# Optimization experiments

Hardware: AMD Instinct MI355X
Metric: run time of the kernel (lower is better)

## Reference

```python
import jax, jax.numpy as jnp
import numpy as np

B = 65536   # batch
S = 3       # pad_size / seq len
DIN = 72    # input feature dim
D = 100     # dim_model
H = 10      # num_head
DH = D // H # dim_head = 10
FF = 512    # ffn hidden
L = 8       # encoder layers
CLS = 40    # cls_dim


def _pos_encoding():
    pe = np.array([[pos / 10000.0 ** (i // 2 * 2.0 / D) for i in range(D)]
                   for pos in range(S)], dtype=np.float32)
    pe[:, 0::2] = np.sin(pe[:, 0::2])
    pe[:, 1::2] = np.cos(pe[:, 1::2])
    return jnp.asarray(pe)  # [S, D]


def setup_inputs() -> dict:
    key = jax.random.key(0)
    ks = jax.random.split(key, 24)
    n = lambda k, shape: 0.05 * jax.random.normal(k, shape, dtype=jnp.float32)
    inp = {
        'x': jax.random.normal(ks[0], (B, S, DIN), dtype=jnp.float32),
        'label': jax.random.randint(ks[1], (B,), 0, CLS),
        'fa_label': jax.random.randint(ks[2], (B,), 0, CLS),
        'We': n(ks[3], (D, DIN)), 'be': n(ks[4], (D,)),
        'pe': _pos_encoding(),
        'Wq': n(ks[5], (L, D, D)), 'bq': n(ks[6], (L, D)),
        'Wk': n(ks[7], (L, D, D)), 'bk': n(ks[8], (L, D)),
        'Wv': n(ks[9], (L, D, D)), 'bv': n(ks[10], (L, D)),
        'Wo': n(ks[11], (L, D, D)), 'bo': n(ks[12], (L, D)),
        'ln1_g': jnp.ones((L, D), jnp.float32), 'ln1_b': jnp.zeros((L, D), jnp.float32),
        'W1': n(ks[13], (L, FF, D)), 'b1': n(ks[14], (L, FF)),
        'W2': n(ks[15], (L, D, FF)), 'b2': n(ks[16], (L, D)),
        'ln2_g': jnp.ones((L, D), jnp.float32), 'ln2_b': jnp.zeros((L, D), jnp.float32),
        'Wf': n(ks[17], (CLS, S * D)), 'bf': n(ks[18], (CLS,)),
    }
    return inp


def _ln(x, g, b, eps=1e-5):
    m = x.mean(-1, keepdims=True)
    v = ((x - m) ** 2).mean(-1, keepdims=True)
    return (x - m) / jnp.sqrt(v + eps) * g + b


def _forward(x, We, be, pe, Wq, bq, Wk, bk, Wv, bv, Wo, bo,
             ln1_g, ln1_b, W1, b1, W2, b2, ln2_g, ln2_b, Wf, bf):
    Bsz = x.shape[0]
    out = x @ We.T + be          # [B, S, D] embedding
    out = out + pe               # positional encoding (dropout = identity in eval)
    scale = DH ** -0.5
    for i in range(L):
        xin = out
        Q = xin @ Wq[i].T + bq[i]
        K = xin @ Wk[i].T + bk[i]
        V = xin @ Wv[i].T + bv[i]
        # Faithful row-major reshape (original uses .view, which interleaves
        # seq and head dims rather than a transpose-based head split).
        Qh = Q.reshape(Bsz * H, -1, DH)   # [B*H, S, DH]
        Kh = K.reshape(Bsz * H, -1, DH)
        Vh = V.reshape(Bsz * H, -1, DH)
        attn = jax.nn.softmax(jnp.einsum('bqd,bkd->bqk', Qh, Kh) * scale, axis=-1)
        ctx = jnp.einsum('bqk,bkd->bqd', attn, Vh).reshape(Bsz, -1, D)
        out = _ln(ctx @ Wo[i].T + bo[i] + xin, ln1_g[i], ln1_b[i])
        # position-wise FFN
        h = jax.nn.relu(out @ W1[i].T + b1[i])
        out = _ln(h @ W2[i].T + b2[i] + out, ln2_g[i], ln2_b[i])
    out = out.reshape(Bsz, S * D) @ Wf.T + bf   # [B, CLS]
    return out


def reference(x, label, fa_label, We, be, pe, Wq, bq, Wk, bk, Wv, bv, Wo, bo,
              ln1_g, ln1_b, W1, b1, W2, b2, ln2_g, ln2_b, Wf, bf):
    # label / fa_label are unused in the original forward
    return _forward(x, We, be, pe, Wq, bq, Wk, bk, Wv, bv, Wo, bo,
                    ln1_g, ln1_b, W1, b1, W2, b2, ln2_g, ln2_b, Wf, bf)
```

## Files before the change

kernel.cpp:

```cpp
#include <hip/hip_runtime.h>
#include <hip/hip_bf16.h>


typedef __attribute__((ext_vector_type(8))) short short8;
typedef __attribute__((ext_vector_type(4))) float floatx4;

namespace {
constexpr int S = 3, DIN = 72, D = 100, FF = 512, L = 8, CLS = 40;
constexpr int NB = 16, R = 48, NT = 256;
constexpr int LDA = 136;
constexpr int LDH = 200;
constexpr float SCALE_L2E = 0.45622024f;

constexpr int PL_QKVO = 7 * 4 * 512;
constexpr int WQ_OFF = 0;
constexpr int WK_OFF = WQ_OFF + L * PL_QKVO;
constexpr int WV_OFF = WK_OFF + L * PL_QKVO;
constexpr int WO_OFF = WV_OFF + L * PL_QKVO;
constexpr int PL_W1 = 32 * 4 * 512;
constexpr int W1_OFF = WO_OFF + L * PL_QKVO;
constexpr int PL_W2 = 7 * 16 * 512;
constexpr int W2_OFF = W1_OFF + L * PL_W1;
constexpr int WE_OFF = W2_OFF + L * PL_W2;
}

__device__ __forceinline__ unsigned short f2bf(float f) {
  unsigned int u = __float_as_uint(f);
  u = u + 0x7fffu + ((u >> 16) & 1u);
  return (unsigned short)(u >> 16);
}

__device__ __forceinline__ unsigned pkbf(float a, float b) {
  __hip_bfloat162 h = __float22bfloat162_rn(make_float2(a, b));
  return *reinterpret_cast<unsigned*>(&h);
}

__device__ __forceinline__ void st_bf4(unsigned short* p, floatx4 v) {
  *reinterpret_cast<uint2*>(p) = make_uint2(pkbf(v.x, v.y), pkbf(v.z, v.w));
}

__device__ __forceinline__ void load10(float* o, const unsigned short* p) {
  const unsigned* u = (const unsigned*)p;
#pragma unroll
  for (int w = 0; w < 5; ++w) {
    unsigned x = u[w];
    o[2 * w] = __uint_as_float(x << 16);
    o[2 * w + 1] = __uint_as_float(x & 0xffff0000u);
  }
}

__device__ __forceinline__ void ldwf4(const unsigned short* base, short8* o) {
#pragma unroll
  for (int ks = 0; ks < 4; ++ks) o[ks] = *(const short8*)(base + ks * 512);
}

__device__ __forceinline__ void ln_rows(float* xrow, const float* srow,
                                        const float* __restrict__ g,
                                        const float* __restrict__ b,
                                        unsigned short* sArow, int ln,
                                        int cnt) {
  floatx4 v[7];
  float sum = 0.f;
#pragma unroll
  for (int i = 0; i < 7; ++i)
    if (i < cnt) {
      const int col = i * 16 + ln * 4;
      floatx4 t = *(const floatx4*)(xrow + col) + *(const floatx4*)(srow + col);
      v[i] = t;
      sum += t.x + t.y + t.z + t.w;
    }
  sum += __shfl_xor(sum, 1, 4);
  sum += __shfl_xor(sum, 2, 4);
  const float mean = sum * 0.01f;
  float var = 0.f;
#pragma unroll
  for (int i = 0; i < 7; ++i)
    if (i < cnt) {
      floatx4 d = v[i] - mean;
      var += d.x * d.x + d.y * d.y + d.z * d.z + d.w * d.w;
    }
  var += __shfl_xor(var, 1, 4);
  var += __shfl_xor(var, 2, 4);
  const float rstd = rsqrtf(var * 0.01f + 1e-5f);
#pragma unroll
  for (int i = 0; i < 7; ++i)
    if (i < cnt) {
      const int col = i * 16 + ln * 4;
      floatx4 o = (v[i] - mean) * rstd * *(const floatx4*)(g + col) +
                  *(const floatx4*)(b + col);
      *(floatx4*)(xrow + col) = o;
      st_bf4(sArow + col, o);
    }
}

__global__ void prep_weights(const float* __restrict__ Wq, const float* __restrict__ Wk,
                             const float* __restrict__ Wv, const float* __restrict__ Wo,
                             const float* __restrict__ W1, const float* __restrict__ W2,
                             const float* __restrict__ We,
                             unsigned short* __restrict__ ws) {
  const int gid = blockIdx.x * 256 + threadIdx.x;
  constexpr int T_QKVO = 8 * 7 * 4 * 64;
  constexpr int T_W1 = 8 * 32 * 4 * 64;
  constexpr int T_W2 = 8 * 7 * 16 * 64;
  constexpr int T_WE = 7 * 3 * 64;
  if (gid >= 4 * T_QKVO + T_W1 + T_W2 + T_WE) return;

  const float* src;
  unsigned short* dst;
  int within, ntc, ksc, N, Ksrc, lstride;
  if (gid < 4 * T_QKVO) {
    const int t = gid / T_QKVO;
    within = gid % T_QKVO;
    src = (t == 0 ? Wq : t == 1 ? Wk : t == 2 ? Wv : Wo);
    dst = ws + (t == 0 ? WQ_OFF : t == 1 ? WK_OFF : t == 2 ? WV_OFF : WO_OFF);
    ntc = 7; ksc = 4; N = 100; Ksrc = 100; lstride = 10000;
  } else if (gid < 4 * T_QKVO + T_W1) {
    within = gid - 4 * T_QKVO;
    src = W1; dst = ws + W1_OFF;
    ntc = 32; ksc = 4; N = 512; Ksrc = 100; lstride = 51200;
  } else if (gid < 4 * T_QKVO + T_W1 + T_W2) {
    within = gid - 4 * T_QKVO - T_W1;
    src = W2; dst = ws + W2_OFF;
    ntc = 7; ksc = 16; N = 100; Ksrc = 512; lstride = 51200;
  } else {
    within = gid - 4 * T_QKVO - T_W1 - T_W2;
    src = We; dst = ws + WE_OFF;
    ntc = 7; ksc = 3; N = 100; Ksrc = 72; lstride = 0;
  }
  const int lane = within & 63;
  int tmp = within >> 6;
  const int ks = tmp % ksc; tmp /= ksc;
  const int nt = tmp % ntc;
  const int lay = tmp / ntc;
  const int n = nt * 16 + (lane & 15);
  const int kb = ks * 32 + (lane >> 4) * 8;
  const float* sp = src + (size_t)lay * lstride + (size_t)n * Ksrc;
  unsigned short o[8];
#pragma unroll
  for (int j = 0; j < 8; ++j) {
    const int k = kb + j;
    float v = (n < N && k < Ksrc) ? sp[k] : 0.f;
    o[j] = f2bf(v);
  }
  uint4 pk = make_uint4((unsigned)o[0] | ((unsigned)o[1] << 16),
                        (unsigned)o[2] | ((unsigned)o[3] << 16),
                        (unsigned)o[4] | ((unsigned)o[5] << 16),
                        (unsigned)o[6] | ((unsigned)o[7] << 16));
  *reinterpret_cast<uint4*>(dst + (size_t)within * 8) = pk;
}

__global__ __launch_bounds__(NT, 3)
void geomap_mfma(const float* __restrict__ gx,
                 const float* __restrict__ be, const float* __restrict__ pe,
                 const float* __restrict__ bq, const float* __restrict__ bk,
                 const float* __restrict__ bv, const float* __restrict__ bo,
                 const float* __restrict__ g1, const float* __restrict__ bt1,
                 const float* __restrict__ b1, const float* __restrict__ b2,
                 const float* __restrict__ g2, const float* __restrict__ bt2,
                 const float* __restrict__ Wf, const float* __restrict__ bfc,
                 const unsigned short* __restrict__ ws,
                 float* __restrict__ gout) {
  __shared__ __align__(16) char smem[51456];
  unsigned short* sA = (unsigned short*)smem;
  float* sXf = (float*)(smem + 13056);
  unsigned short* sQ = (unsigned short*)(smem + 32256);
  unsigned short* sK = (unsigned short*)(smem + 41856);
  float* scr = (float*)(smem + 32256);
  unsigned short* sH = (unsigned short*)(smem + 32256);

  const int tid = threadIdx.x;
  const int lane = tid & 63;
  const int wid = tid >> 6;
  const int l15 = lane & 15;
  const int quad = lane >> 4;
  const int blk = blockIdx.x;

  const int row_o = tid >> 2, ln_o = tid & 3;
  const int cnt_o = (ln_o == 0) ? 7 : 6;

  for (int i = tid; i < R * LDA / 2; i += NT) ((unsigned*)sA)[i] = 0u;
  __syncthreads();
  for (int i = tid; i < R * DIN / 2; i += NT) {
    const int row = i / 36, c = (i % 36) * 2;
    const float2 f2 = *(const float2*)(gx + ((size_t)blk * R + row) * DIN + c);
    ((unsigned*)sA)[row * (LDA / 2) + (c >> 1)] = pkbf(f2.x, f2.y);
  }
  __syncthreads();

  {
    short8 xe[3][3];
#pragma unroll
    for (int mt = 0; mt < 3; ++mt)
#pragma unroll
      for (int ks = 0; ks < 3; ++ks)
        xe[mt][ks] = *(const short8*)(sA + (mt * 16 + l15) * LDA + ks * 32 + quad * 8);
    __syncthreads();
    for (int nt = wid; nt < 7; nt += 4) {
      const unsigned short* wb = ws + WE_OFF + (size_t)(nt * 3) * 512 + (size_t)lane * 8;
      short8 w0 = *(const short8*)(wb);
      short8 w1 = *(const short8*)(wb + 512);
      short8 w2 = *(const short8*)(wb + 1024);
      const int n0 = nt * 16 + quad * 4;
      floatx4 a[3];
      __builtin_amdgcn_s_setprio(1);
#pragma unroll
      for (int mt = 0; mt < 3; ++mt) {
        a[mt] = floatx4{0.f, 0.f, 0.f, 0.f};
        a[mt] = __builtin_amdgcn_mfma_f32_16x16x32_bf16(w0, xe[mt][0], a[mt], 0, 0, 0);
        a[mt] = __builtin_amdgcn_mfma_f32_16x16x32_bf16(w1, xe[mt][1], a[mt], 0, 0, 0);
        a[mt] = __builtin_amdgcn_mfma_f32_16x16x32_bf16(w2, xe[mt][2], a[mt], 0, 0, 0);
      }
      __builtin_amdgcn_s_setprio(0);
      if (n0 < D) {
        const floatx4 bev = *(const floatx4*)(be + n0);
#pragma unroll
        for (int mt = 0; mt < 3; ++mt) {
          const int row = mt * 16 + l15;
          const int s = row % 3;
          const floatx4 pev = *(const floatx4*)(pe + s * D + n0);
          const floatx4 o = a[mt] + bev + pev;
          *(floatx4*)(sXf + row * D + n0) = o;
          st_bf4(sA + row * LDA + n0, o);
        }
      }
    }
  }
  __syncthreads();

  for (int lay = 0; lay < L; ++lay) {
    {
      short8 xf[3][4];
#pragma unroll
      for (int mt = 0; mt < 3; ++mt)
#pragma unroll
        for (int ks = 0; ks < 4; ++ks)
          xf[mt][ks] = *(const short8*)(sA + (mt * 16 + l15) * LDA + ks * 32 + quad * 8);
      __syncthreads();
      const unsigned short* wbase[3] = {ws + WQ_OFF + lay * PL_QKVO,
                                        ws + WK_OFF + lay * PL_QKVO,
                                        ws + WV_OFF + lay * PL_QKVO};
      for (int u = wid; u < 21; u += 4) {
        const int mat = u / 7, nt = u % 7;
        short8 wf[4];
        ldwf4(wbase[mat] + (size_t)nt * 2048 + (size_t)lane * 8, wf);
        const int n0 = nt * 16 + quad * 4;
        floatx4 bias = {0.f, 0.f, 0.f, 0.f};
        const float* bsrc = (mat == 0 ? bq : mat == 1 ? bk : bv) + lay * D;
        if (n0 < D) bias = *(const floatx4*)(bsrc + n0);
        floatx4 a0 = bias, a1 = bias, a2 = bias;
        __builtin_amdgcn_s_setprio(1);
#pragma unroll
        for (int ks = 0; ks < 4; ++ks) {
          a0 = __builtin_amdgcn_mfma_f32_16x16x32_bf16(wf[ks], xf[0][ks], a0, 0, 0, 0);
          a1 = __builtin_amdgcn_mfma_f32_16x16x32_bf16(wf[ks], xf[1][ks], a1, 0, 0, 0);
          a2 = __builtin_amdgcn_mfma_f32_16x16x32_bf16(wf[ks], xf[2][ks], a2, 0, 0, 0);
        }
        __builtin_amdgcn_s_setprio(0);
        if (n0 < D) {
          const floatx4 av[3] = {a0, a1, a2};
#pragma unroll
          for (int mt = 0; mt < 3; ++mt) {
            const int row = mt * 16 + l15;
            if (mat == 0) st_bf4(sQ + row * 100 + n0, av[mt]);
            else if (mat == 1) st_bf4(sK + row * 100 + n0, av[mt]);
            else st_bf4(sA + row * LDA + n0, av[mt]);
          }
        }
      }
    }
    __syncthreads();

    if (tid < 160) {
      const int e = tid / 10, h = tid % 10;
      const unsigned short* Qe = sQ + e * 300;
      const unsigned short* Ke = sK + e * 300;
      float Kv[3][10];
#pragma unroll
      for (int t = 0; t < 3; ++t) load10(Kv[t], Ke + h * 30 + t * 10);
      float p[3][3];
#pragma unroll
      for (int sq = 0; sq < 3; ++sq) {
        float q[10];
        load10(q, Qe + h * 30 + sq * 10);
        float sc[3];
#pragma unroll
        for (int t = 0; t < 3; ++t) {
          float s0 = 0.f;
#pragma unroll
          for (int j = 0; j < 10; ++j) s0 += q[j] * Kv[t][j];
          sc[t] = s0 * SCALE_L2E;
        }
        const float m = fmaxf(sc[0], fmaxf(sc[1], sc[2]));
        float p0 = exp2f(sc[0] - m), p1 = exp2f(sc[1] - m), p2 = exp2f(sc[2] - m);
        const float inv = 1.f / (p0 + p1 + p2);
        p[sq][0] = p0 * inv; p[sq][1] = p1 * inv; p[sq][2] = p2 * inv;
      }
      float ctx[3][10];
#pragma unroll
      for (int sq = 0; sq < 3; ++sq)
#pragma unroll
        for (int j = 0; j < 10; ++j) ctx[sq][j] = 0.f;
#pragma unroll
      for (int t = 0; t < 3; ++t) {
        const int pv = h * 30 + t * 10;
        float vv[10];
        load10(vv, sA + (e * 3 + pv / 100) * LDA + (pv % 100));
#pragma unroll
        for (int sq = 0; sq < 3; ++sq)
#pragma unroll
          for (int j = 0; j < 10; ++j) ctx[sq][j] += p[sq][t] * vv[j];
      }
#pragma unroll
      for (int sq = 0; sq < 3; ++sq) {
        const int pq = h * 30 + sq * 10;
        unsigned* dp = (unsigned*)(sA + (e * 3 + pq / 100) * LDA + (pq % 100));
#pragma unroll
        for (int w = 0; w < 5; ++w)
          dp[w] = pkbf(ctx[sq][2 * w], ctx[sq][2 * w + 1]);
      }
    }
    __syncthreads();

    {
      short8 cf[3][4];
#pragma unroll
      for (int mt = 0; mt < 3; ++mt)
#pragma unroll
        for (int ks = 0; ks < 4; ++ks)
          cf[mt][ks] = *(const short8*)(sA + (mt * 16 + l15) * LDA + ks * 32 + quad * 8);
      const unsigned short* wbase = ws + WO_OFF + lay * PL_QKVO;
      for (int u = wid; u < 7; u += 4) {
        short8 wf[4];
        ldwf4(wbase + (size_t)u * 2048 + (size_t)lane * 8, wf);
        const int n0 = u * 16 + quad * 4;
        floatx4 bias = {0.f, 0.f, 0.f, 0.f};
        if (n0 < D) bias = *(const floatx4*)(bo + lay * D + n0);
        floatx4 a0 = bias, a1 = bias, a2 = bias;
        __builtin_amdgcn_s_setprio(1);
#pragma unroll
        for (int ks = 0; ks < 4; ++ks) {
          a0 = __builtin_amdgcn_mfma_f32_16x16x32_bf16(wf[ks], cf[0][ks], a0, 0, 0, 0);
          a1 = __builtin_amdgcn_mfma_f32_16x16x32_bf16(wf[ks], cf[1][ks], a1, 0, 0, 0);
          a2 = __builtin_amdgcn_mfma_f32_16x16x32_bf16(wf[ks], cf[2][ks], a2, 0, 0, 0);
        }
        __builtin_amdgcn_s_setprio(0);
        if (n0 < D) {
          const floatx4 av[3] = {a0, a1, a2};
#pragma unroll
          for (int mt = 0; mt < 3; ++mt)
            *(floatx4*)(scr + (mt * 16 + l15) * D + n0) = av[mt];
        }
      }
    }
    __syncthreads();
    if (tid < 192)
      ln_rows(sXf + row_o * D, scr + row_o * D, g1 + lay * D, bt1 + lay * D,
              sA + row_o * LDA, ln_o, cnt_o);
    __syncthreads();

    {
      short8 ff[3][4];
#pragma unroll
      for (int mt = 0; mt < 3; ++mt)
#pragma unroll
        for (int ks = 0; ks < 4; ++ks)
          ff[mt][ks] = *(const short8*)(sA + (mt * 16 + l15) * LDA + ks * 32 + quad * 8);
      floatx4 facc[2][3];
      const int ntA = wid, ntB = wid + 4;
#pragma unroll
      for (int idx = 0; idx < 2; ++idx) {
        const int nt = idx == 0 ? ntA : ntB;
        const int n0 = nt * 16 + quad * 4;
        floatx4 bias = {0.f, 0.f, 0.f, 0.f};
        if (nt < 7 && n0 < D) bias = *(const floatx4*)(b2 + lay * D + n0);
#pragma unroll
        for (int mt = 0; mt < 3; ++mt) facc[idx][mt] = bias;
      }
      const unsigned short* w1b = ws + W1_OFF + (size_t)lay * PL_W1;
      const unsigned short* w2b = ws + W2_OFF + (size_t)lay * PL_W2;

#pragma unroll
      for (int c = 0; c < 3; ++c) {
        const int base_nt = c * 12;
        const int cnt_nt = (c == 2) ? 8 : 12;
        const int kb = c * 6, ke = kb + ((c == 2) ? 4 : 6);
        for (int l = wid; l < cnt_nt; l += 4) {
          const int ntg = base_nt + l;
          short8 wf[4];
          ldwf4(w1b + (size_t)ntg * 2048 + (size_t)lane * 8, wf);
          const floatx4 b1v = *(const floatx4*)(b1 + lay * FF + ntg * 16 + quad * 4);
          floatx4 a0 = b1v, a1 = b1v, a2 = b1v;
          __builtin_amdgcn_s_setprio(1);
#pragma unroll
          for (int ks = 0; ks < 4; ++ks) {
            a0 = __builtin_amdgcn_mfma_f32_16x16x32_bf16(wf[ks], ff[0][ks], a0, 0, 0, 0);
            a1 = __builtin_amdgcn_mfma_f32_16x16x32_bf16(wf[ks], ff[1][ks], a1, 0, 0, 0);
            a2 = __builtin_amdgcn_mfma_f32_16x16x32_bf16(wf[ks], ff[2][ks], a2, 0, 0, 0);
          }
          __builtin_amdgcn_s_setprio(0);
          const int nloc = l * 16 + quad * 4;
          const floatx4 av[3] = {a0, a1, a2};
#pragma unroll
          for (int mt = 0; mt < 3; ++mt) {
            const int row = mt * 16 + l15;
            floatx4 r;
            r.x = fmaxf(av[mt].x, 0.f); r.y = fmaxf(av[mt].y, 0.f);
            r.z = fmaxf(av[mt].z, 0.f); r.w = fmaxf(av[mt].w, 0.f);
            st_bf4(sH + row * LDH + nloc, r);
          }
        }
        __syncthreads();
        short8 wA = *(const short8*)(w2b + (size_t)(ntA * 16 + kb) * 512 + (size_t)lane * 8);
        short8 wB = wA;
        if (ntB < 7)
          wB = *(const short8*)(w2b + (size_t)(ntB * 16 + kb) * 512 + (size_t)lane * 8);
        for (int ksl = kb; ksl < ke; ++ksl) {
          short8 nA = wA, nB = wB;
          if (ksl + 1 < ke) {
            nA = *(const short8*)(w2b + (size_t)(ntA * 16 + ksl + 1) * 512 + (size_t)lane * 8);
            if (ntB < 7)
              nB = *(const short8*)(w2b + (size_t)(ntB * 16 + ksl + 1) * 512 + (size_t)lane * 8);
          }
          short8 hf[3];
#pragma unroll
          for (int mt = 0; mt < 3; ++mt)
            hf[mt] = *(const short8*)(sH + (mt * 16 + l15) * LDH + (ksl - kb) * 32 + quad * 8);
          __builtin_amdgcn_s_setprio(1);
#pragma unroll
          for (int mt = 0; mt < 3; ++mt)
            facc[0][mt] = __builtin_amdgcn_mfma_f32_16x16x32_bf16(wA, hf[mt], facc[0][mt], 0, 0, 0);
          if (ntB < 7) {
#pragma unroll
            for (int mt = 0; mt < 3; ++mt)
              facc[1][mt] = __builtin_amdgcn_mfma_f32_16x16x32_bf16(wB, hf[mt], facc[1][mt], 0, 0, 0);
          }
          __builtin_amdgcn_s_setprio(0);
          wA = nA; wB = nB;
        }
        __syncthreads();
      }
#pragma unroll
      for (int idx = 0; idx < 2; ++idx) {
        const int nt = idx == 0 ? ntA : ntB;
        const int n0 = nt * 16 + quad * 4;
        if (nt < 7 && n0 < D) {
#pragma unroll
          for (int mt = 0; mt < 3; ++mt)
            *(floatx4*)(scr + (mt * 16 + l15) * D + n0) = facc[idx][mt];
        }
      }
    }
    __syncthreads();
    if (tid < 192)
      ln_rows(sXf + row_o * D, scr + row_o * D, g2 + lay * D, bt2 + lay * D,
              sA + row_o * LDA, ln_o, cnt_o);
    __syncthreads();
  }

  if (tid < 160) {
    const int c = tid % 40, eg = tid / 40;
    float acc[4];
#pragma unroll
    for (int i = 0; i < 4; ++i) acc[i] = bfc[c];
    const floatx4* wr = (const floatx4*)(Wf + c * 300);
    for (int kq = 0; kq < 75; ++kq) {
      const floatx4 w4 = wr[kq];
#pragma unroll
      for (int i = 0; i < 4; ++i) {
        const floatx4 x4 = *(const floatx4*)(sXf + (eg * 4 + i) * 300 + kq * 4);
        acc[i] += w4.x * x4.x + w4.y * x4.y + w4.z * x4.z + w4.w * x4.w;
      }
    }
#pragma unroll
    for (int i = 0; i < 4; ++i)
      gout[((size_t)blk * NB + eg * 4 + i) * CLS + c] = acc[i];
  }
}

extern "C" void kernel_launch(void* const* d_in, const int* in_sizes, int n_in,
                              void* d_out, int out_size, void* d_ws,
                              size_t ws_size, hipStream_t stream) {
  const float* x   = (const float*)d_in[0];
  const float* We  = (const float*)d_in[3];
  const float* be  = (const float*)d_in[4];
  const float* pe  = (const float*)d_in[5];
  const float* Wq  = (const float*)d_in[6];
  const float* bq  = (const float*)d_in[7];
  const float* Wk  = (const float*)d_in[8];
  const float* bk  = (const float*)d_in[9];
  const float* Wv  = (const float*)d_in[10];
  const float* bv  = (const float*)d_in[11];
  const float* Wo  = (const float*)d_in[12];
  const float* bo  = (const float*)d_in[13];
  const float* g1  = (const float*)d_in[14];
  const float* bt1 = (const float*)d_in[15];
  const float* W1  = (const float*)d_in[16];
  const float* b1  = (const float*)d_in[17];
  const float* W2  = (const float*)d_in[18];
  const float* b2  = (const float*)d_in[19];
  const float* g2  = (const float*)d_in[20];
  const float* bt2 = (const float*)d_in[21];
  const float* Wf  = (const float*)d_in[22];
  const float* bf  = (const float*)d_in[23];
  float* out = (float*)d_out;
  unsigned short* ws = (unsigned short*)d_ws;

  prep_weights<<<710, 256, 0, stream>>>(Wq, Wk, Wv, Wo, W1, W2, We, ws);

  const int B = in_sizes[0] / (S * DIN);
  const int blocks = B / NB;
  geomap_mfma<<<blocks, NT, 0, stream>>>(x, be, pe, bq, bk, bv, bo,
                                         g1, bt1, b1, b2, g2, bt2, Wf, bf,
                                         ws, out);
}
```

Before: 1.201 ms.

## Software-pipeline FFN with double-buffered hidden tiles overlapping FFN1 and FFN2

The FFN is restructured from three chunks into a seven-phase pipeline over six 96-column hidden chunks, using two ping-pong LDS buffers. In each phase the FFN1 (W1+ReLU) output for chunk p is written into one buffer while the FFN2 (W2) accumulation reads the previous chunk from the other. This halves the barriers per chunk, since each phase needs one sync instead of two, and interleaves the two GEMM stages. It also prefetches W1 and W2 fragments ahead of use. The cost is more live registers and more complex control flow, and the last-chunk handling is irregular.

Result: slower. 1.405 ms (+17.0%).

```diff
diff --git a/kernel.cpp b/kernel.cpp
--- a/kernel.cpp
+++ b/kernel.cpp
@@ -9,7 +9,6 @@
 constexpr int S = 3, DIN = 72, D = 100, FF = 512, L = 8, CLS = 40;
 constexpr int NB = 16, R = 48, NT = 256;
 constexpr int LDA = 136;
-constexpr int LDH = 200;
 constexpr float SCALE_L2E = 0.45622024f;
 
 constexpr int PL_QKVO = 7 * 4 * 512;
@@ -23,6 +22,8 @@
 constexpr int W2_OFF = W1_OFF + L * PL_W1;
 constexpr int WE_OFF = W2_OFF + L * PL_W2;
 }
+
+#define MFMA_BF16 __builtin_amdgcn_mfma_f32_16x16x32_bf16
 
 __device__ __forceinline__ unsigned short f2bf(float f) {
   unsigned int u = __float_as_uint(f);
@@ -206,9 +207,9 @@
 #pragma unroll
       for (int mt = 0; mt < 3; ++mt) {
         a[mt] = floatx4{0.f, 0.f, 0.f, 0.f};
-        a[mt] = __builtin_amdgcn_mfma_f32_16x16x32_bf16(w0, xe[mt][0], a[mt], 0, 0, 0);
-        a[mt] = __builtin_amdgcn_mfma_f32_16x16x32_bf16(w1, xe[mt][1], a[mt], 0, 0, 0);
-        a[mt] = __builtin_amdgcn_mfma_f32_16x16x32_bf16(w2, xe[mt][2], a[mt], 0, 0, 0);
+        a[mt] = MFMA_BF16(w0, xe[mt][0], a[mt], 0, 0, 0);
+        a[mt] = MFMA_BF16(w1, xe[mt][1], a[mt], 0, 0, 0);
+        a[mt] = MFMA_BF16(w2, xe[mt][2], a[mt], 0, 0, 0);
       }
       __builtin_amdgcn_s_setprio(0);
       if (n0 < D) {
@@ -251,9 +252,9 @@
         __builtin_amdgcn_s_setprio(1);
 #pragma unroll
         for (int ks = 0; ks < 4; ++ks) {
-          a0 = __builtin_amdgcn_mfma_f32_16x16x32_bf16(wf[ks], xf[0][ks], a0, 0, 0, 0);
-          a1 = __builtin_amdgcn_mfma_f32_16x16x32_bf16(wf[ks], xf[1][ks], a1, 0, 0, 0);
-          a2 = __builtin_amdgcn_mfma_f32_16x16x32_bf16(wf[ks], xf[2][ks], a2, 0, 0, 0);
+          a0 = MFMA_BF16(wf[ks], xf[0][ks], a0, 0, 0, 0);
+          a1 = MFMA_BF16(wf[ks], xf[1][ks], a1, 0, 0, 0);
+          a2 = MFMA_BF16(wf[ks], xf[2][ks], a2, 0, 0, 0);
         }
         __builtin_amdgcn_s_setprio(0);
         if (n0 < D) {
@@ -339,9 +340,9 @@
         __builtin_amdgcn_s_setprio(1);
 #pragma unroll
         for (int ks = 0; ks < 4; ++ks) {
-          a0 = __builtin_amdgcn_mfma_f32_16x16x32_bf16(wf[ks], cf[0][ks], a0, 0, 0, 0);
-          a1 = __builtin_amdgcn_mfma_f32_16x16x32_bf16(wf[ks], cf[1][ks], a1, 0, 0, 0);
-          a2 = __builtin_amdgcn_mfma_f32_16x16x32_bf16(wf[ks], cf[2][ks], a2, 0, 0, 0);
+          a0 = MFMA_BF16(wf[ks], cf[0][ks], a0, 0, 0, 0);
+          a1 = MFMA_BF16(wf[ks], cf[1][ks], a1, 0, 0, 0);
+          a2 = MFMA_BF16(wf[ks], cf[2][ks], a2, 0, 0, 0);
         }
         __builtin_amdgcn_s_setprio(0);
         if (n0 < D) {
@@ -367,6 +368,7 @@
           ff[mt][ks] = *(const short8*)(sA + (mt * 16 + l15) * LDA + ks * 32 + quad * 8);
       floatx4 facc[2][3];
       const int ntA = wid, ntB = wid + 4;
+      const bool hasB2 = ntB < 7;
 #pragma unroll
       for (int idx = 0; idx < 2; ++idx) {
         const int nt = idx == 0 ? ntA : ntB;
@@ -378,67 +380,127 @@
       }
       const unsigned short* w1b = ws + W1_OFF + (size_t)lay * PL_W1;
       const unsigned short* w2b = ws + W2_OFF + (size_t)lay * PL_W2;
-
-#pragma unroll
-      for (int c = 0; c < 3; ++c) {
-        const int base_nt = c * 12;
-        const int cnt_nt = (c == 2) ? 8 : 12;
-        const int kb = c * 6, ke = kb + ((c == 2) ? 4 : 6);
-        for (int l = wid; l < cnt_nt; l += 4) {
-          const int ntg = base_nt + l;
-          short8 wf[4];
-          ldwf4(w1b + (size_t)ntg * 2048 + (size_t)lane * 8, wf);
-          const floatx4 b1v = *(const floatx4*)(b1 + lay * FF + ntg * 16 + quad * 4);
-          floatx4 a0 = b1v, a1 = b1v, a2 = b1v;
-          __builtin_amdgcn_s_setprio(1);
-#pragma unroll
-          for (int ks = 0; ks < 4; ++ks) {
-            a0 = __builtin_amdgcn_mfma_f32_16x16x32_bf16(wf[ks], ff[0][ks], a0, 0, 0, 0);
-            a1 = __builtin_amdgcn_mfma_f32_16x16x32_bf16(wf[ks], ff[1][ks], a1, 0, 0, 0);
-            a2 = __builtin_amdgcn_mfma_f32_16x16x32_bf16(wf[ks], ff[2][ks], a2, 0, 0, 0);
+      unsigned short* const bufA = sH;
+      unsigned short* const bufB = sH + 48 * 96;
+
+#define FFN1_UNIT(W0, W1_, W2_, W3, NTG, LC)                               \
+  do {                                                                     \
+    const floatx4 _bv =                                                    \
+        *(const floatx4*)(b1 + lay * FF + (NTG) * 16 + quad * 4);          \
+    floatx4 _a0 = _bv, _a1 = _bv, _a2 = _bv;                               \
+    __builtin_amdgcn_s_setprio(1);                                         \
+    _a0 = MFMA_BF16(W0, ff[0][0], _a0, 0, 0, 0);                           \
+    _a1 = MFMA_BF16(W0, ff[1][0], _a1, 0, 0, 0);                           \
+    _a2 = MFMA_BF16(W0, ff[2][0], _a2, 0, 0, 0);                           \
+    _a0 = MFMA_BF16(W1_, ff[0][1], _a0, 0, 0, 0);                          \
+    _a1 = MFMA_BF16(W1_, ff[1][1], _a1, 0, 0, 0);                          \
+    _a2 = MFMA_BF16(W1_, ff[2][1], _a2, 0, 0, 0);                          \
+    _a0 = MFMA_BF16(W2_, ff[0][2], _a0, 0, 0, 0);                          \
+    _a1 = MFMA_BF16(W2_, ff[1][2], _a1, 0, 0, 0);                          \
+    _a2 = MFMA_BF16(W2_, ff[2][2], _a2, 0, 0, 0);                          \
+    _a0 = MFMA_BF16(W3, ff[0][3], _a0, 0, 0, 0);                           \
+    _a1 = MFMA_BF16(W3, ff[1][3], _a1, 0, 0, 0);                           \
+    _a2 = MFMA_BF16(W3, ff[2][3], _a2, 0, 0, 0);                           \
+    __builtin_amdgcn_s_setprio(0);                                         \
+    const int _nc = (LC) + quad * 4;                                       \
+    floatx4 _r;                                                            \
+    _r.x = fmaxf(_a0.x, 0.f); _r.y = fmaxf(_a0.y, 0.f);                    \
+    _r.z = fmaxf(_a0.z, 0.f); _r.w = fmaxf(_a0.w, 0.f);                    \
+    st_bf4(wbuf + (l15) * 96 + _nc, _r);                                   \
+    _r.x = fmaxf(_a1.x, 0.f); _r.y = fmaxf(_a1.y, 0.f);                    \
+    _r.z = fmaxf(_a1.z, 0.f); _r.w = fmaxf(_a1.w, 0.f);                    \
+    st_bf4(wbuf + (16 + l15) * 96 + _nc, _r);                              \
+    _r.x = fmaxf(_a2.x, 0.f); _r.y = fmaxf(_a2.y, 0.f);                    \
+    _r.z = fmaxf(_a2.z, 0.f); _r.w = fmaxf(_a2.w, 0.f);                    \
+    st_bf4(wbuf + (32 + l15) * 96 + _nc, _r);                              \
+  } while (0)
+
+#define FFN2_STEP(WA, WB, KSL)                                             \
+  do {                                                                     \
+    const int _ko = (KSL) * 32 + quad * 8;                                 \
+    short8 _h0 = *(const short8*)(rbuf + (l15) * 96 + _ko);                \
+    short8 _h1 = *(const short8*)(rbuf + (16 + l15) * 96 + _ko);           \
+    short8 _h2 = *(const short8*)(rbuf + (32 + l15) * 96 + _ko);           \
+    __builtin_amdgcn_s_setprio(1);                                         \
+    facc[0][0] = MFMA_BF16(WA, _h0, facc[0][0], 0, 0, 0);                  \
+    facc[0][1] = MFMA_BF16(WA, _h1, facc[0][1], 0, 0, 0);                  \
+    facc[0][2] = MFMA_BF16(WA, _h2, facc[0][2], 0, 0, 0);                  \
+    if (hasB2) {                                                           \
+      facc[1][0] = MFMA_BF16(WB, _h0, facc[1][0], 0, 0, 0);                \
+      facc[1][1] = MFMA_BF16(WB, _h1, facc[1][1], 0, 0, 0);                \
+      facc[1][2] = MFMA_BF16(WB, _h2, facc[1][2], 0, 0, 0);                \
+    }                                                                      \
+    __builtin_amdgcn_s_setprio(0);                                         \
+  } while (0)
+
+#pragma unroll
+      for (int p = 0; p < 7; ++p) {
+        unsigned short* const wbuf = (p & 1) ? bufB : bufA;
+        const unsigned short* const rbuf = (p & 1) ? bufA : bufB;
+        const int la = (p == 5) ? (wid & 1) : wid;
+        const bool aOK = (p != 5) || (wid < 2);
+        const bool bOn = (p < 6) && (p != 5) && (wid < 2);
+        short8 fa0, fa1, fa2, fa3, fb0, fb1, fb2, fb3;
+        if (p < 6) {
+          const unsigned short* pa =
+              w1b + (size_t)(p * 6 + la) * 2048 + (size_t)lane * 8;
+          fa0 = *(const short8*)(pa);
+          fa1 = *(const short8*)(pa + 512);
+          fa2 = *(const short8*)(pa + 1024);
+          fa3 = *(const short8*)(pa + 1536);
+          if (bOn) {
+            const unsigned short* pb =
+                w1b + (size_t)(p * 6 + wid + 4) * 2048 + (size_t)lane * 8;
+            fb0 = *(const short8*)(pb);
+            fb1 = *(const short8*)(pb + 512);
+            fb2 = *(const short8*)(pb + 1024);
+            fb3 = *(const short8*)(pb + 1536);
           }
-          __builtin_amdgcn_s_setprio(0);
-          const int nloc = l * 16 + quad * 4;
-          const floatx4 av[3] = {a0, a1, a2};
-#pragma unroll
-          for (int mt = 0; mt < 3; ++mt) {
-            const int row = mt * 16 + l15;
-            floatx4 r;
-            r.x = fmaxf(av[mt].x, 0.f); r.y = fmaxf(av[mt].y, 0.f);
-            r.z = fmaxf(av[mt].z, 0.f); r.w = fmaxf(av[mt].w, 0.f);
-            st_bf4(sH + row * LDH + nloc, r);
+        }
+        if (p == 0) {
+          FFN1_UNIT(fa0, fa1, fa2, fa3, wid, wid * 16);
+          if (bOn)
+            FFN1_UNIT(fb0, fb1, fb2, fb3, wid + 4, (wid + 4) * 16);
+        } else {
+          const int q = p - 1;
+          short8 wA0 = *(const short8*)(w2b + (size_t)(ntA * 16 + q * 3) * 512 +
+                                        (size_t)lane * 8);
+          short8 wB0 = wA0;
+          if (hasB2)
+            wB0 = *(const short8*)(w2b + (size_t)(ntB * 16 + q * 3) * 512 +
+                                   (size_t)lane * 8);
+          if (p < 6 && aOK)
+            FFN1_UNIT(fa0, fa1, fa2, fa3, p * 6 + la, la * 16);
+          if (q < 5) {
+            short8 wA1 = *(const short8*)(w2b +
+                                          (size_t)(ntA * 16 + q * 3 + 1) * 512 +
+                                          (size_t)lane * 8);
+            short8 wB1 = wA1;
+            if (hasB2)
+              wB1 = *(const short8*)(w2b +
+                                     (size_t)(ntB * 16 + q * 3 + 1) * 512 +
+                                     (size_t)lane * 8);
+            FFN2_STEP(wA0, wB0, 0);
+            if (bOn)
+              FFN1_UNIT(fb0, fb1, fb2, fb3, p * 6 + wid + 4, (wid + 4) * 16);
+            short8 wA2 = *(const short8*)(w2b +
+                                          (size_t)(ntA * 16 + q * 3 + 2) * 512 +
+                                          (size_t)lane * 8);
+            short8 wB2 = wA2;
+            if (hasB2)
+              wB2 = *(const short8*)(w2b +
+                                     (size_t)(ntB * 16 + q * 3 + 2) * 512 +
+                                     (size_t)lane * 8);
+            FFN2_STEP(wA1, wB1, 1);
+            FFN2_STEP(wA2, wB2, 2);
+          } else {
+            FFN2_STEP(wA0, wB0, 0);
           }
         }
         __syncthreads();
-        short8 wA = *(const short8*)(w2b + (size_t)(ntA * 16 + kb) * 512 + (size_t)lane * 8);
-        short8 wB = wA;
-        if (ntB < 7)
-          wB = *(const short8*)(w2b + (size_t)(ntB * 16 + kb) * 512 + (size_t)lane * 8);
-        for (int ksl = kb; ksl < ke; ++ksl) {
-          short8 nA = wA, nB = wB;
-          if (ksl + 1 < ke) {
-            nA = *(const short8*)(w2b + (size_t)(ntA * 16 + ksl + 1) * 512 + (size_t)lane * 8);
-            if (ntB < 7)
-              nB = *(const short8*)(w2b + (size_t)(ntB * 16 + ksl + 1) * 512 + (size_t)lane * 8);
-          }
-          short8 hf[3];
-#pragma unroll
-          for (int mt = 0; mt < 3; ++mt)
-            hf[mt] = *(const short8*)(sH + (mt * 16 + l15) * LDH + (ksl - kb) * 32 + quad * 8);
-          __builtin_amdgcn_s_setprio(1);
-#pragma unroll
-          for (int mt = 0; mt < 3; ++mt)
-            facc[0][mt] = __builtin_amdgcn_mfma_f32_16x16x32_bf16(wA, hf[mt], facc[0][mt], 0, 0, 0);
-          if (ntB < 7) {
-#pragma unroll
-            for (int mt = 0; mt < 3; ++mt)
-              facc[1][mt] = __builtin_amdgcn_mfma_f32_16x16x32_bf16(wB, hf[mt], facc[1][mt], 0, 0, 0);
-          }
-          __builtin_amdgcn_s_setprio(0);
-          wA = nA; wB = nB;
-        }
-        __syncthreads();
-      }
+      }
+#undef FFN1_UNIT
+#undef FFN2_STEP
 #pragma unroll
       for (int idx = 0; idx < 2; ++idx) {
         const int nt = idx == 0 ? ntA : ntB;
```

## Software-pipeline FFN with double-buffered hidden chunks overlapping W1 and W2 GEMMs

Applied to the files above, without the earlier changes.

Restructures the FFN so the 512-wide hidden layer is produced in 8 chunks of 64 columns into two small ping-pong LDS buffers. Each step computes the next W1 chunk while the W2 accumulation consumes the previous chunk, which is meant to overlap the two GEMMs and cut the number of barriers. It also shrinks the LDS hidden buffer, which could raise occupancy. The cost is more complex control flow and higher register pressure from holding both weight sets live at once.

After: 1.290 ms. 1.07x slower.

```diff
diff --git a/kernel.cpp b/kernel.cpp
--- a/kernel.cpp
+++ b/kernel.cpp
@@ -9,7 +9,7 @@
 constexpr int S = 3, DIN = 72, D = 100, FF = 512, L = 8, CLS = 40;
 constexpr int NB = 16, R = 48, NT = 256;
 constexpr int LDA = 136;
-constexpr int LDH = 200;
+constexpr int LDF = 72;
 constexpr float SCALE_L2E = 0.45622024f;
 
 constexpr int PL_QKVO = 7 * 4 * 512;
@@ -23,6 +23,8 @@
 constexpr int W2_OFF = W1_OFF + L * PL_W1;
 constexpr int WE_OFF = W2_OFF + L * PL_W2;
 }
+
+#define MFMA_BF16 __builtin_amdgcn_mfma_f32_16x16x32_bf16
 
 __device__ __forceinline__ unsigned short f2bf(float f) {
   unsigned int u = __float_as_uint(f);
@@ -206,9 +208,9 @@
 #pragma unroll
       for (int mt = 0; mt < 3; ++mt) {
         a[mt] = floatx4{0.f, 0.f, 0.f, 0.f};
-        a[mt] = __builtin_amdgcn_mfma_f32_16x16x32_bf16(w0, xe[mt][0], a[mt], 0, 0, 0);
-        a[mt] = __builtin_amdgcn_mfma_f32_16x16x32_bf16(w1, xe[mt][1], a[mt], 0, 0, 0);
-        a[mt] = __builtin_amdgcn_mfma_f32_16x16x32_bf16(w2, xe[mt][2], a[mt], 0, 0, 0);
+        a[mt] = MFMA_BF16(w0, xe[mt][0], a[mt], 0, 0, 0);
+        a[mt] = MFMA_BF16(w1, xe[mt][1], a[mt], 0, 0, 0);
+        a[mt] = MFMA_BF16(w2, xe[mt][2], a[mt], 0, 0, 0);
       }
       __builtin_amdgcn_s_setprio(0);
       if (n0 < D) {
@@ -251,9 +253,9 @@
         __builtin_amdgcn_s_setprio(1);
 #pragma unroll
         for (int ks = 0; ks < 4; ++ks) {
-          a0 = __builtin_amdgcn_mfma_f32_16x16x32_bf16(wf[ks], xf[0][ks], a0, 0, 0, 0);
-          a1 = __builtin_amdgcn_mfma_f32_16x16x32_bf16(wf[ks], xf[1][ks], a1, 0, 0, 0);
-          a2 = __builtin_amdgcn_mfma_f32_16x16x32_bf16(wf[ks], xf[2][ks], a2, 0, 0, 0);
+          a0 = MFMA_BF16(wf[ks], xf[0][ks], a0, 0, 0, 0);
+          a1 = MFMA_BF16(wf[ks], xf[1][ks], a1, 0, 0, 0);
+          a2 = MFMA_BF16(wf[ks], xf[2][ks], a2, 0, 0, 0);
         }
         __builtin_amdgcn_s_setprio(0);
         if (n0 < D) {
@@ -339,9 +341,9 @@
         __builtin_amdgcn_s_setprio(1);
 #pragma unroll
         for (int ks = 0; ks < 4; ++ks) {
-          a0 = __builtin_amdgcn_mfma_f32_16x16x32_bf16(wf[ks], cf[0][ks], a0, 0, 0, 0);
-          a1 = __builtin_amdgcn_mfma_f32_16x16x32_bf16(wf[ks], cf[1][ks], a1, 0, 0, 0);
-          a2 = __builtin_amdgcn_mfma_f32_16x16x32_bf16(wf[ks], cf[2][ks], a2, 0, 0, 0);
+          a0 = MFMA_BF16(wf[ks], cf[0][ks], a0, 0, 0, 0);
+          a1 = MFMA_BF16(wf[ks], cf[1][ks], a1, 0, 0, 0);
+          a2 = MFMA_BF16(wf[ks], cf[2][ks], a2, 0, 0, 0);
         }
         __builtin_amdgcn_s_setprio(0);
         if (n0 < D) {
@@ -367,6 +369,7 @@
           ff[mt][ks] = *(const short8*)(sA + (mt * 16 + l15) * LDA + ks * 32 + quad * 8);
       floatx4 facc[2][3];
       const int ntA = wid, ntB = wid + 4;
+      const bool hasB2 = ntB < 7;
 #pragma unroll
       for (int idx = 0; idx < 2; ++idx) {
         const int nt = idx == 0 ? ntA : ntB;
@@ -378,67 +381,113 @@
       }
       const unsigned short* w1b = ws + W1_OFF + (size_t)lay * PL_W1;
       const unsigned short* w2b = ws + W2_OFF + (size_t)lay * PL_W2;
-
-#pragma unroll
-      for (int c = 0; c < 3; ++c) {
-        const int base_nt = c * 12;
-        const int cnt_nt = (c == 2) ? 8 : 12;
-        const int kb = c * 6, ke = kb + ((c == 2) ? 4 : 6);
-        for (int l = wid; l < cnt_nt; l += 4) {
-          const int ntg = base_nt + l;
-          short8 wf[4];
-          ldwf4(w1b + (size_t)ntg * 2048 + (size_t)lane * 8, wf);
-          const floatx4 b1v = *(const floatx4*)(b1 + lay * FF + ntg * 16 + quad * 4);
-          floatx4 a0 = b1v, a1 = b1v, a2 = b1v;
-          __builtin_amdgcn_s_setprio(1);
-#pragma unroll
-          for (int ks = 0; ks < 4; ++ks) {
-            a0 = __builtin_amdgcn_mfma_f32_16x16x32_bf16(wf[ks], ff[0][ks], a0, 0, 0, 0);
-            a1 = __builtin_amdgcn_mfma_f32_16x16x32_bf16(wf[ks], ff[1][ks], a1, 0, 0, 0);
-            a2 = __builtin_amdgcn_mfma_f32_16x16x32_bf16(wf[ks], ff[2][ks], a2, 0, 0, 0);
-          }
-          __builtin_amdgcn_s_setprio(0);
-          const int nloc = l * 16 + quad * 4;
-          const floatx4 av[3] = {a0, a1, a2};
-#pragma unroll
-          for (int mt = 0; mt < 3; ++mt) {
-            const int row = mt * 16 + l15;
-            floatx4 r;
-            r.x = fmaxf(av[mt].x, 0.f); r.y = fmaxf(av[mt].y, 0.f);
-            r.z = fmaxf(av[mt].z, 0.f); r.w = fmaxf(av[mt].w, 0.f);
-            st_bf4(sH + row * LDH + nloc, r);
-          }
-        }
+      unsigned short* const bufA = sH;
+      unsigned short* const bufB = sH + 48 * LDF;
+
+      auto f1_unit = [&](short8 u0, short8 u1, short8 u2, short8 u3, int gu,
+                         unsigned short* wbuf) {
+        const floatx4 b1v =
+            *(const floatx4*)(b1 + lay * FF + gu * 16 + quad * 4);
+        floatx4 a0 = b1v, a1 = b1v, a2 = b1v;
+        __builtin_amdgcn_s_setprio(1);
+        a0 = MFMA_BF16(u0, ff[0][0], a0, 0, 0, 0);
+        a1 = MFMA_BF16(u0, ff[1][0], a1, 0, 0, 0);
+        a2 = MFMA_BF16(u0, ff[2][0], a2, 0, 0, 0);
+        a0 = MFMA_BF16(u1, ff[0][1], a0, 0, 0, 0);
+        a1 = MFMA_BF16(u1, ff[1][1], a1, 0, 0, 0);
+        a2 = MFMA_BF16(u1, ff[2][1], a2, 0, 0, 0);
+        a0 = MFMA_BF16(u2, ff[0][2], a0, 0, 0, 0);
+        a1 = MFMA_BF16(u2, ff[1][2], a1, 0, 0, 0);
+        a2 = MFMA_BF16(u2, ff[2][2], a2, 0, 0, 0);
+        a0 = MFMA_BF16(u3, ff[0][3], a0, 0, 0, 0);
+        a1 = MFMA_BF16(u3, ff[1][3], a1, 0, 0, 0);
+        a2 = MFMA_BF16(u3, ff[2][3], a2, 0, 0, 0);
+        __builtin_amdgcn_s_setprio(0);
+        const int nc = wid * 16 + quad * 4;
+        floatx4 r;
+        r.x = fmaxf(a0.x, 0.f); r.y = fmaxf(a0.y, 0.f);
+        r.z = fmaxf(a0.z, 0.f); r.w = fmaxf(a0.w, 0.f);
+        st_bf4(wbuf + l15 * LDF + nc, r);
+        r.x = fmaxf(a1.x, 0.f); r.y = fmaxf(a1.y, 0.f);
+        r.z = fmaxf(a1.z, 0.f); r.w = fmaxf(a1.w, 0.f);
+        st_bf4(wbuf + (16 + l15) * LDF + nc, r);
+        r.x = fmaxf(a2.x, 0.f); r.y = fmaxf(a2.y, 0.f);
+        r.z = fmaxf(a2.z, 0.f); r.w = fmaxf(a2.w, 0.f);
+        st_bf4(wbuf + (32 + l15) * LDF + nc, r);
+      };
+      auto f2_step = [&](short8 wA, short8 wB, const unsigned short* rbuf,
+                         int kl) {
+        const int ko = kl * 32 + quad * 8;
+        short8 h0 = *(const short8*)(rbuf + l15 * LDF + ko);
+        short8 h1 = *(const short8*)(rbuf + (16 + l15) * LDF + ko);
+        short8 h2 = *(const short8*)(rbuf + (32 + l15) * LDF + ko);
+        __builtin_amdgcn_s_setprio(1);
+        facc[0][0] = MFMA_BF16(wA, h0, facc[0][0], 0, 0, 0);
+        facc[0][1] = MFMA_BF16(wA, h1, facc[0][1], 0, 0, 0);
+        facc[0][2] = MFMA_BF16(wA, h2, facc[0][2], 0, 0, 0);
+        if (hasB2) {
+          facc[1][0] = MFMA_BF16(wB, h0, facc[1][0], 0, 0, 0);
+          facc[1][1] = MFMA_BF16(wB, h1, facc[1][1], 0, 0, 0);
+          facc[1][2] = MFMA_BF16(wB, h2, facc[1][2], 0, 0, 0);
+        }
+        __builtin_amdgcn_s_setprio(0);
+      };
+
+      {
+        const unsigned short* pa = w1b + (size_t)wid * 2048 + (size_t)lane * 8;
+        short8 u0 = *(const short8*)(pa);
+        short8 u1 = *(const short8*)(pa + 512);
+        short8 u2 = *(const short8*)(pa + 1024);
+        short8 u3 = *(const short8*)(pa + 1536);
+        f1_unit(u0, u1, u2, u3, wid, bufA);
+      }
+      __syncthreads();
+#pragma unroll 1
+      for (int p = 1; p < 8; ++p) {
+        unsigned short* const wbuf = (p & 1) ? bufB : bufA;
+        const unsigned short* const rbuf = (p & 1) ? bufA : bufB;
+        const int q = p - 1;
+        const int gu = p * 4 + wid;
+        const unsigned short* pa = w1b + (size_t)gu * 2048 + (size_t)lane * 8;
+        short8 u0 = *(const short8*)(pa);
+        short8 u1 = *(const short8*)(pa + 512);
+        short8 u2 = *(const short8*)(pa + 1024);
+        short8 u3 = *(const short8*)(pa + 1536);
+        short8 wA0 = *(const short8*)(w2b + (size_t)(ntA * 16 + q * 2) * 512 +
+                                      (size_t)lane * 8);
+        short8 wB0 = wA0;
+        if (hasB2)
+          wB0 = *(const short8*)(w2b + (size_t)(ntB * 16 + q * 2) * 512 +
+                                 (size_t)lane * 8);
+        f2_step(wA0, wB0, rbuf, 0);
+        short8 wA1 = *(const short8*)(w2b +
+                                      (size_t)(ntA * 16 + q * 2 + 1) * 512 +
+                                      (size_t)lane * 8);
+        short8 wB1 = wA1;
+        if (hasB2)
+          wB1 = *(const short8*)(w2b + (size_t)(ntB * 16 + q * 2 + 1) * 512 +
+                                 (size_t)lane * 8);
+        f1_unit(u0, u1, u2, u3, gu, wbuf);
+        f2_step(wA1, wB1, rbuf, 1);
         __syncthreads();
-        short8 wA = *(const short8*)(w2b + (size_t)(ntA * 16 + kb) * 512 + (size_t)lane * 8);
-        short8 wB = wA;
-        if (ntB < 7)
-          wB = *(const short8*)(w2b + (size_t)(ntB * 16 + kb) * 512 + (size_t)lane * 8);
-        for (int ksl = kb; ksl < ke; ++ksl) {
-          short8 nA = wA, nB = wB;
-          if (ksl + 1 < ke) {
-            nA = *(const short8*)(w2b + (size_t)(ntA * 16 + ksl + 1) * 512 + (size_t)lane * 8);
-            if (ntB < 7)
-              nB = *(const short8*)(w2b + (size_t)(ntB * 16 + ksl + 1) * 512 + (size_t)lane * 8);
-          }
-          short8 hf[3];
-#pragma unroll
-          for (int mt = 0; mt < 3; ++mt)
-            hf[mt] = *(const short8*)(sH + (mt * 16 + l15) * LDH + (ksl - kb) * 32 + quad * 8);
-          __builtin_amdgcn_s_setprio(1);
-#pragma unroll
-          for (int mt = 0; mt < 3; ++mt)
-            facc[0][mt] = __builtin_amdgcn_mfma_f32_16x16x32_bf16(wA, hf[mt], facc[0][mt], 0, 0, 0);
-          if (ntB < 7) {
-#pragma unroll
-            for (int mt = 0; mt < 3; ++mt)
-              facc[1][mt] = __builtin_amdgcn_mfma_f32_16x16x32_bf16(wB, hf[mt], facc[1][mt], 0, 0, 0);
-          }
-          __builtin_amdgcn_s_setprio(0);
-          wA = nA; wB = nB;
-        }
-        __syncthreads();
-      }
+      }
+      {
+        short8 wA0 = *(const short8*)(w2b + (size_t)(ntA * 16 + 14) * 512 +
+                                      (size_t)lane * 8);
+        short8 wB0 = wA0;
+        if (hasB2)
+          wB0 = *(const short8*)(w2b + (size_t)(ntB * 16 + 14) * 512 +
+                                 (size_t)lane * 8);
+        short8 wA1 = *(const short8*)(w2b + (size_t)(ntA * 16 + 15) * 512 +
+                                      (size_t)lane * 8);
+        short8 wB1 = wA1;
+        if (hasB2)
+          wB1 = *(const short8*)(w2b + (size_t)(ntB * 16 + 15) * 512 +
+                                 (size_t)lane * 8);
+        f2_step(wA0, wB0, bufB, 0);
+        f2_step(wA1, wB1, bufB, 1);
+      }
+      __syncthreads();
 #pragma unroll
       for (int idx = 0; idx < 2; ++idx) {
         const int nt = idx == 0 ? ntA : ntB;
```
